# Optimization experiments

Hardware: AMD Instinct MI355X
Metric: run time of the kernel (lower is better)

The kernel has to match this reference:

```python
import jax, jax.numpy as jnp
import numpy as np

VOCAB = 10000
KEY_SIZE = 256
VALUE_SIZE = 256
HIDDEN = KEY_SIZE + VALUE_SIZE  # 512, embedding dim (tied with output head)
SOS = 33


def _lstm_cell(x, h, c, W_ih, W_hh, b_ih, b_hh):
    # torch.nn.LSTMCell: gates = x@W_ih^T + b_ih + h@W_hh^T + b_hh, order i,f,g,o
    g = x @ W_ih.T + b_ih + h @ W_hh.T + b_hh
    i, f, gg, o = jnp.split(g, 4, axis=1)
    c_new = jax.nn.sigmoid(f) * c + jax.nn.sigmoid(i) * jnp.tanh(gg)
    h_new = jax.nn.sigmoid(o) * jnp.tanh(c_new)
    return h_new, c_new


def _attend(q, K, V, invalid):
    # q: [N,H]; K: [N,T,H]; V: [N,T,Vd]; invalid: [N,T] bool mask of padded positions
    energy = jnp.einsum('nth,nh->nt', K, q)
    energy = jnp.where(invalid, jnp.float32(-1e10), energy)
    attn = jax.nn.softmax(energy, axis=1)
    ctx = jnp.einsum('nt,ntv->nv', attn, V)
    return ctx


def setup_inputs() -> dict:
    key0 = jax.random.key(0)
    ks = jax.random.split(key0, 16)
    N, T, L = 64, 512, 256
    values = jax.random.normal(ks[0], (N, T, VALUE_SIZE), dtype=jnp.float32)
    key = jax.random.normal(ks[1], (N, T, KEY_SIZE), dtype=jnp.float32)
    lens = jax.random.randint(ks[2], (N,), 64, T + 1, dtype=jnp.int32)
    text = jax.random.randint(ks[3], (N, L), 0, VOCAB, dtype=jnp.int32)
    s = 1.0 / np.sqrt(KEY_SIZE)
    E = jax.random.normal(ks[4], (VOCAB, HIDDEN), dtype=jnp.float32) * 0.02
    b_out = jnp.zeros((VOCAB,), dtype=jnp.float32)
    W_ih1 = jax.random.uniform(ks[5], (4 * KEY_SIZE, HIDDEN + VALUE_SIZE), jnp.float32, -s, s)
    W_hh1 = jax.random.uniform(ks[6], (4 * KEY_SIZE, KEY_SIZE), jnp.float32, -s, s)
    b_ih1 = jax.random.uniform(ks[7], (4 * KEY_SIZE,), jnp.float32, -s, s)
    b_hh1 = jax.random.uniform(ks[8], (4 * KEY_SIZE,), jnp.float32, -s, s)
    W_ih2 = jax.random.uniform(ks[9], (4 * KEY_SIZE, KEY_SIZE), jnp.float32, -s, s)
    W_hh2 = jax.random.uniform(ks[10], (4 * KEY_SIZE, KEY_SIZE), jnp.float32, -s, s)
    b_ih2 = jax.random.uniform(ks[11], (4 * KEY_SIZE,), jnp.float32, -s, s)
    b_hh2 = jax.random.uniform(ks[12], (4 * KEY_SIZE,), jnp.float32, -s, s)
    return {"values": values, "key": key, "lens": lens, "text": text,
            "E": E, "b_out": b_out,
            "W_ih1": W_ih1, "W_hh1": W_hh1, "b_ih1": b_ih1, "b_hh1": b_hh1,
            "W_ih2": W_ih2, "W_hh2": W_hh2, "b_ih2": b_ih2, "b_hh2": b_hh2}


def reference(values, key, lens, text, E, b_out,
              W_ih1, W_hh1, b_ih1, b_hh1, W_ih2, W_hh2, b_ih2, b_hh2):
    # isAttended=True, isTrain=True, teacher_force_rate=1.0 -> always teacher forcing.
    N, T, _ = values.shape
    L = text.shape[1]
    invalid = jnp.arange(T)[None, :] >= lens[:, None]  # [N,T] padded positions

    # char embeddings fed at each step: step 0 uses <sos>=33, step i>0 uses text[:, i-1]
    emb = E[text]                                   # [N,L,H]
    first = jnp.broadcast_to(E[SOS][None, :], (N, HIDDEN))
    emb_seq = jnp.concatenate([first[None], jnp.swapaxes(emb, 0, 1)[:-1]], axis=0)  # [L,N,H]

    ctx0 = _attend(jnp.zeros((N, KEY_SIZE), values.dtype), key, values, invalid)
    h1 = jnp.zeros((N, KEY_SIZE), values.dtype)
    carry0 = (h1, h1, h1, h1, ctx0)  # (h1,c1,h2,c2,context)

    def step(carry, char_embed):
        h1, c1, h2, c2, ctx = carry
        inp = jnp.concatenate([char_embed, ctx], axis=1)   # [N, H+V]
        h1, c1 = _lstm_cell(inp, h1, c1, W_ih1, W_hh1, b_ih1, b_hh1)
        h2, c2 = _lstm_cell(h1, h2, c2, W_ih2, W_hh2, b_ih2, b_hh2)
        ctx = _attend(h2, key, values, invalid)
        logits = jnp.concatenate([h2, ctx], axis=1) @ E.T + b_out  # tied weights
        return (h1, c1, h2, c2, ctx), logits

    _, preds = jax.lax.scan(step, carry0, emb_seq)  # [L,N,VOCAB]
    return jnp.transpose(preds, (1, 0, 2))          # [N,L,VOCAB]
```

## Files before the change

kernel.cpp:

```cpp
#include <hip/hip_runtime.h>
#include <hip/hip_bf16.h>
#include <math.h>

#define NB     64
#define TT     512
#define KS     256
#define VS     256
#define HID    512
#define GATES  1024
#define LL     256
#define VOC    10000
#define SOSTOK 33

__device__ __forceinline__ float sigmoidf_(float x) { return 1.0f / (1.0f + expf(-x)); }

__global__ __launch_bounds__(256)
void pack_kernel(const float* __restrict__ W_ih1, const float* __restrict__ W_hh1,
                 const float* __restrict__ b_ih1, const float* __restrict__ b_hh1,
                 const float* __restrict__ W_ih2, const float* __restrict__ W_hh2,
                 const float* __restrict__ b_ih2, const float* __restrict__ b_hh2,
                 float* __restrict__ W1T, float* __restrict__ W2T,
                 float* __restrict__ b1s, float* __restrict__ b2s)
{
    int idx = blockIdx.x * 256 + threadIdx.x;
    if (idx < 512 * 1024) {
        int k = idx >> 10;
        int j = idx & 1023;
        W1T[idx] = (k < 256) ? W_ih1[j * 768 + 512 + k] : W_hh1[j * 256 + (k - 256)];
        W2T[idx] = (k < 256) ? W_ih2[j * 256 + k]       : W_hh2[j * 256 + (k - 256)];
    }
    if (idx < 1024) {
        b1s[idx] = b_ih1[idx] + b_hh1[idx];
        b2s[idx] = b_ih2[idx] + b_hh2[idx];
    }
}

template <int MODE>
__global__ __launch_bounds__(256)
void gemm_nt(const float* __restrict__ A, const float* __restrict__ B,
             float* __restrict__ C, const float* __restrict__ bias,
             int M, int Nn, int K, int lda, int ldb, int ldc)
{
    const int BM = 128, BN = 128, BK = 16;
    __shared__ float As[BK][BM + 4];
    __shared__ float Bs[BK][BN + 4];

    const int m0 = blockIdx.y * BM;
    const int n0 = blockIdx.x * BN;
    const int tid = threadIdx.x;
    const int tx = tid & 15;
    const int ty = tid >> 4;
    const int lr = tid >> 2;
    const int lq = tid & 3;

    float acc[8][8];
#pragma unroll
    for (int i = 0; i < 8; i++)
#pragma unroll
        for (int j = 0; j < 8; j++) acc[i][j] = 0.0f;

    for (int k0 = 0; k0 < K; k0 += BK) {
#pragma unroll
        for (int h = 0; h < 2; h++) {
            int r = lr + h * 64;
            int gm = m0 + r;
            float4 v = make_float4(0.f, 0.f, 0.f, 0.f);
            if (gm < M) v = *(const float4*)(A + (size_t)gm * lda + k0 + lq * 4);
            As[lq * 4 + 0][r] = v.x; As[lq * 4 + 1][r] = v.y;
            As[lq * 4 + 2][r] = v.z; As[lq * 4 + 3][r] = v.w;
        }
#pragma unroll
        for (int h = 0; h < 2; h++) {
            int r = lr + h * 64;
            int gn = n0 + r;
            float4 v = make_float4(0.f, 0.f, 0.f, 0.f);
            if (gn < Nn) v = *(const float4*)(B + (size_t)gn * ldb + k0 + lq * 4);
            Bs[lq * 4 + 0][r] = v.x; Bs[lq * 4 + 1][r] = v.y;
            Bs[lq * 4 + 2][r] = v.z; Bs[lq * 4 + 3][r] = v.w;
        }
        __syncthreads();

#pragma unroll
        for (int kk = 0; kk < BK; kk++) {
            float a[8], b[8];
            *(float4*)&a[0] = *(const float4*)&As[kk][ty * 4];
            *(float4*)&a[4] = *(const float4*)&As[kk][64 + ty * 4];
            *(float4*)&b[0] = *(const float4*)&Bs[kk][tx * 4];
            *(float4*)&b[4] = *(const float4*)&Bs[kk][64 + tx * 4];
#pragma unroll
            for (int i = 0; i < 8; i++)
#pragma unroll
                for (int j = 0; j < 8; j++) acc[i][j] += a[i] * b[j];
        }
        __syncthreads();
    }

    int row[8];
#pragma unroll
    for (int i = 0; i < 8; i++) row[i] = m0 + ((i < 4) ? (ty * 4 + i) : (64 + ty * 4 + (i - 4)));
    const int c0 = n0 + tx * 4;
    const int c1 = n0 + 64 + tx * 4;

    if (MODE == 0) {
#pragma unroll
        for (int i = 0; i < 8; i++) {
            if (row[i] >= M) continue;
            float* cp = C + (size_t)row[i] * ldc;
#pragma unroll
            for (int jh = 0; jh < 2; jh++) {
                int cc = jh ? c1 : c0;
                if (cc + 3 < Nn) {
                    *(float4*)(cp + cc) = make_float4(acc[i][jh * 4 + 0], acc[i][jh * 4 + 1],
                                                      acc[i][jh * 4 + 2], acc[i][jh * 4 + 3]);
                } else {
                    for (int j = 0; j < 4; j++)
                        if (cc + j < Nn) cp[cc + j] = acc[i][jh * 4 + j];
                }
            }
        }
    } else {
        float bv0[4], bv1[4];
#pragma unroll
        for (int j = 0; j < 4; j++) {
            bv0[j] = (c0 + j < Nn) ? bias[c0 + j] : 0.f;
            bv1[j] = (c1 + j < Nn) ? bias[c1 + j] : 0.f;
        }
#pragma unroll
        for (int i = 0; i < 8; i++) {
            int m = row[i];
            int t = m >> 6;
            int nb = m & 63;
            float* cp = C + ((size_t)nb * LL + t) * VOC;
#pragma unroll
            for (int jh = 0; jh < 2; jh++) {
                int cc = jh ? c1 : c0;
                float* bv = jh ? bv1 : bv0;
                if (cc + 3 < Nn) {
                    *(float4*)(cp + cc) = make_float4(acc[i][jh * 4 + 0] + bv[0],
                                                      acc[i][jh * 4 + 1] + bv[1],
                                                      acc[i][jh * 4 + 2] + bv[2],
                                                      acc[i][jh * 4 + 3] + bv[3]);
                } else {
                    for (int j = 0; j < 4; j++)
                        if (cc + j < Nn) cp[cc + j] = acc[i][jh * 4 + j] + bv[j];
                }
            }
        }
    }
}

__global__ __launch_bounds__(256)
void seq_kernel(const float* __restrict__ Vmat,
                const float* __restrict__ Kmat,
                const int* __restrict__ lens,
                const int* __restrict__ text,
                const float* __restrict__ preE,
                const float* __restrict__ W1T,
                const float* __restrict__ W2T,
                const float* __restrict__ b1s,
                const float* __restrict__ b2s,
                float* __restrict__ S)
{
    const int n = blockIdx.x;
    const int tid = threadIdx.x;

    __shared__ float h1[KS], c1v[KS], h2[KS], c2v[KS], ctx[VS];
    __shared__ float xv[512];
    __shared__ float attn[TT];
    __shared__ float red[256];

    const int len = lens[n];
    const float* Kn = Kmat + (size_t)n * TT * KS;
    const float* Vn = Vmat + (size_t)n * TT * VS;

    h1[tid] = 0.f; c1v[tid] = 0.f; h2[tid] = 0.f; c2v[tid] = 0.f;
    __syncthreads();

    auto attention = [&]() {
        float e0 = -1e10f, e1 = -1e10f;
        {
            int t = tid;
            if (t < len) {
                const float4* kr = (const float4*)(Kn + (size_t)t * KS);
                float acc = 0.f;
#pragma unroll 8
                for (int k4 = 0; k4 < KS / 4; k4++) {
                    float4 kv = kr[k4];
                    acc += kv.x * h2[k4 * 4 + 0];
                    acc += kv.y * h2[k4 * 4 + 1];
                    acc += kv.z * h2[k4 * 4 + 2];
                    acc += kv.w * h2[k4 * 4 + 3];
                }
                e0 = acc;
            }
            t = tid + 256;
            if (t < len) {
                const float4* kr = (const float4*)(Kn + (size_t)t * KS);
                float acc = 0.f;
#pragma unroll 8
                for (int k4 = 0; k4 < KS / 4; k4++) {
                    float4 kv = kr[k4];
                    acc += kv.x * h2[k4 * 4 + 0];
                    acc += kv.y * h2[k4 * 4 + 1];
                    acc += kv.z * h2[k4 * 4 + 2];
                    acc += kv.w * h2[k4 * 4 + 3];
                }
                e1 = acc;
            }
        }
        red[tid] = fmaxf(e0, e1);
        __syncthreads();
#pragma unroll
        for (int s = 128; s > 0; s >>= 1) {
            if (tid < s) red[tid] = fmaxf(red[tid], red[tid + s]);
            __syncthreads();
        }
        float M = red[0];
        __syncthreads();
        float p0 = expf(e0 - M);
        float p1 = expf(e1 - M);
        attn[tid] = p0; attn[tid + 256] = p1;
        red[tid] = p0 + p1;
        __syncthreads();
#pragma unroll
        for (int s = 128; s > 0; s >>= 1) {
            if (tid < s) red[tid] += red[tid + s];
            __syncthreads();
        }
        float inv = 1.0f / red[0];
        float acc = 0.f;
        const float* vb = Vn + tid;
        for (int t = 0; t < len; t++) acc += attn[t] * vb[(size_t)t * VS];
        ctx[tid] = acc * inv;
        __syncthreads();
    };

    auto lstm = [&](const float* __restrict__ WT, const float* __restrict__ bsum,
                    const float* __restrict__ pre, float* hs, float* cs,
                    const float* xa, const float* xb) {
        xv[tid] = xa[tid];
        xv[256 + tid] = xb[tid];
        __syncthreads();
        float a0 = 0.f, a1 = 0.f, a2 = 0.f, a3 = 0.f;
#pragma unroll 8
        for (int k = 0; k < 512; k++) {
            float x = xv[k];
            const float* wr = WT + (k << 10) + tid;
            a0 += x * wr[0];
            a1 += x * wr[256];
            a2 += x * wr[512];
            a3 += x * wr[768];
        }
        float gi = a0 + bsum[tid];
        float gf = a1 + bsum[tid + 256];
        float gg = a2 + bsum[tid + 512];
        float go = a3 + bsum[tid + 768];
        if (pre) {
            gi += pre[tid];
            gf += pre[tid + 256];
            gg += pre[tid + 512];
            go += pre[tid + 768];
        }
        float c = sigmoidf_(gf) * cs[tid] + sigmoidf_(gi) * tanhf(gg);
        float h = sigmoidf_(go) * tanhf(c);
        __syncthreads();
        hs[tid] = h;
        cs[tid] = c;
        __syncthreads();
    };

    attention();

    for (int t = 0; t < LL; t++) {
        int tok = (t == 0) ? SOSTOK : text[n * LL + (t - 1)];
        lstm(W1T, b1s, preE + (size_t)tok * GATES, h1, c1v, ctx, h1);
        lstm(W2T, b2s, (const float*)nullptr,      h2, c2v, h1, h2);
        attention();
        float* srow = S + ((size_t)t * NB + n) * HID;
        srow[tid] = h2[tid];
        srow[256 + tid] = ctx[tid];
    }
}

extern "C" void kernel_launch(void* const* d_in, const int* in_sizes, int n_in,
                              void* d_out, int out_size, void* d_ws, size_t ws_size,
                              hipStream_t stream)
{
    const float* values = (const float*)d_in[0];
    const float* key    = (const float*)d_in[1];
    const int*   lens   = (const int*)d_in[2];
    const int*   text   = (const int*)d_in[3];
    const float* E      = (const float*)d_in[4];
    const float* b_out  = (const float*)d_in[5];
    const float* W_ih1  = (const float*)d_in[6];
    const float* W_hh1  = (const float*)d_in[7];
    const float* b_ih1  = (const float*)d_in[8];
    const float* b_hh1  = (const float*)d_in[9];
    const float* W_ih2  = (const float*)d_in[10];
    const float* W_hh2  = (const float*)d_in[11];
    const float* b_ih2  = (const float*)d_in[12];
    const float* b_hh2  = (const float*)d_in[13];

    float* ws   = (float*)d_ws;
    float* W1T  = ws;
    float* W2T  = W1T + 524288;
    float* b1s  = W2T + 524288;
    float* b2s  = b1s + 1024;
    float* preE = b2s + 1024;
    float* S    = preE + 10240000;
    float* out  = (float*)d_out;

    hipLaunchKernelGGL(pack_kernel, dim3(2048), dim3(256), 0, stream,
                       W_ih1, W_hh1, b_ih1, b_hh1, W_ih2, W_hh2, b_ih2, b_hh2,
                       W1T, W2T, b1s, b2s);

    hipLaunchKernelGGL((gemm_nt<0>), dim3(8, 79), dim3(256), 0, stream,
                       E, W_ih1, preE, (const float*)nullptr,
                       10000, 1024, 512, 512, 768, 1024);

    hipLaunchKernelGGL(seq_kernel, dim3(64), dim3(256), 0, stream,
                       values, key, lens, text, preE, W1T, W2T, b1s, b2s, S);

    hipLaunchKernelGGL((gemm_nt<1>), dim3(79, 128), dim3(256), 0, stream,
                       S, E, out, b_out,
                       16384, 10000, 512, 512, 512, 0);
}
```

Baseline: 25.88 ms.

## Split sequential decoder across 256 cooperative blocks with group barriers and split-softmax attention

Replaces the 64-block recurrent kernel, one block per batch item, with a 256-block cooperative kernel. Each group of 64 blocks owns 16 batch rows and a slice of LSTM gate columns, and keeps its weight slice resident in shared memory. Attention is split into four time quarters per row and combined with a log-sum-exp merge through global scratch and atomics. The aim is to use far more CUs and stop re-streaming the LSTM weights from global memory every step. In exchange it adds custom global barriers, three per step, and extra global traffic for the h1 and context exchange.

Measured after the change: 49.50 ms. 1.91x slower.

```diff
diff --git a/kernel.cpp b/kernel.cpp
--- a/kernel.cpp
+++ b/kernel.cpp
@@ -1,5 +1,4 @@
 #include <hip/hip_runtime.h>
-#include <hip/hip_bf16.h>
 #include <math.h>
 
 #define NB     64
@@ -12,6 +11,10 @@
 #define VOC    10000
 #define SOSTOK 33
 
+#define NBLK   256
+#define GBLK   64
+#define NTHR   256
+
 __device__ __forceinline__ float sigmoidf_(float x) { return 1.0f / (1.0f + expf(-x)); }
 
 __global__ __launch_bounds__(256)
@@ -19,20 +22,23 @@
                  const float* __restrict__ b_ih1, const float* __restrict__ b_hh1,
                  const float* __restrict__ W_ih2, const float* __restrict__ W_hh2,
                  const float* __restrict__ b_ih2, const float* __restrict__ b_hh2,
-                 float* __restrict__ W1T, float* __restrict__ W2T,
-                 float* __restrict__ b1s, float* __restrict__ b2s)
+                 float* __restrict__ W1c, float* __restrict__ W2c,
+                 float* __restrict__ b1s, float* __restrict__ b2s,
+                 unsigned* __restrict__ cnt, unsigned* __restrict__ bars)
 {
     int idx = blockIdx.x * 256 + threadIdx.x;
-    if (idx < 512 * 1024) {
-        int k = idx >> 10;
-        int j = idx & 1023;
-        W1T[idx] = (k < 256) ? W_ih1[j * 768 + 512 + k] : W_hh1[j * 256 + (k - 256)];
-        W2T[idx] = (k < 256) ? W_ih2[j * 256 + k]       : W_hh2[j * 256 + (k - 256)];
+    if (idx < 1024 * 512) {
+        int j = idx >> 9;
+        int k = idx & 511;
+        W1c[idx] = (k < 256) ? W_ih1[j * 768 + 512 + k] : W_hh1[j * 256 + (k - 256)];
+        W2c[idx] = (k < 256) ? W_ih2[j * 256 + k]       : W_hh2[j * 256 + (k - 256)];
     }
     if (idx < 1024) {
         b1s[idx] = b_ih1[idx] + b_hh1[idx];
         b2s[idx] = b_ih2[idx] + b_hh2[idx];
-    }
+        cnt[idx] = 0u;
+    }
+    if (idx < 256) bars[idx] = 0u;
 }
 
 template <int MODE>
@@ -149,136 +155,256 @@
     }
 }
 
-__global__ __launch_bounds__(256)
-void seq_kernel(const float* __restrict__ Vmat,
-                const float* __restrict__ Kmat,
-                const int* __restrict__ lens,
-                const int* __restrict__ text,
-                const float* __restrict__ preE,
-                const float* __restrict__ W1T,
-                const float* __restrict__ W2T,
-                const float* __restrict__ b1s,
-                const float* __restrict__ b2s,
-                float* __restrict__ S)
+__device__ __forceinline__ void group_sync(unsigned* cntp, unsigned* genp)
 {
-    const int n = blockIdx.x;
+    __threadfence();
+    __syncthreads();
+    if (threadIdx.x == 0) {
+        unsigned g = __hip_atomic_load(genp, __ATOMIC_RELAXED, __HIP_MEMORY_SCOPE_AGENT);
+        unsigned old = __hip_atomic_fetch_add(cntp, 1u, __ATOMIC_RELAXED, __HIP_MEMORY_SCOPE_AGENT);
+        if (old == GBLK - 1) {
+            __hip_atomic_store(cntp, 0u, __ATOMIC_RELAXED, __HIP_MEMORY_SCOPE_AGENT);
+            __hip_atomic_store(genp, g + 1u, __ATOMIC_RELEASE, __HIP_MEMORY_SCOPE_AGENT);
+        } else {
+            unsigned cur;
+            do {
+                __builtin_amdgcn_s_sleep(2);
+                cur = __hip_atomic_load(genp, __ATOMIC_RELAXED, __HIP_MEMORY_SCOPE_AGENT);
+            } while (cur == g);
+        }
+    }
+    __syncthreads();
+    __threadfence();
+}
+
+__global__ __launch_bounds__(256, 1)
+void seq_coop(const float* __restrict__ Vmat,
+              const float* __restrict__ Kmat,
+              const int* __restrict__ lens,
+              const int* __restrict__ text,
+              const float* __restrict__ preE,
+              const float* __restrict__ W1c,
+              const float* __restrict__ W2c,
+              const float* __restrict__ b1s,
+              const float* __restrict__ b2s,
+              float* __restrict__ S,
+              float* __restrict__ h1buf,
+              float* __restrict__ ctxbuf,
+              float* __restrict__ am,
+              float* __restrict__ as_,
+              float* __restrict__ actxp,
+              unsigned* __restrict__ cnt,
+              unsigned* __restrict__ bars)
+{
+    __shared__ float ws1[16][516];
+    __shared__ float ws2[16][516];
+    __shared__ float xs [16][516];
+    __shared__ float gl [16][16];
+    __shared__ float red[256];
+    __shared__ float h2s[256];
+    __shared__ float pl [128];
+    __shared__ float cred[4][64][4];
+    __shared__ int   flagv;
+
+    const int b   = blockIdx.x;
     const int tid = threadIdx.x;
-
-    __shared__ float h1[KS], c1v[KS], h2[KS], c2v[KS], ctx[VS];
-    __shared__ float xv[512];
-    __shared__ float attn[TT];
-    __shared__ float red[256];
-
-    const int len = lens[n];
-    const float* Kn = Kmat + (size_t)n * TT * KS;
-    const float* Vn = Vmat + (size_t)n * TT * VS;
-
-    h1[tid] = 0.f; c1v[tid] = 0.f; h2[tid] = 0.f; c2v[tid] = 0.f;
-    __syncthreads();
-
-    auto attention = [&]() {
-        float e0 = -1e10f, e1 = -1e10f;
+    const int grp = b >> 6;
+    const int n0  = grp * 16;
+    const int ct  = b & 63;
+    const int na  = n0 + ((b >> 2) & 15);
+    const int q   = b & 3;
+    const int t0a = q * 128;
+    unsigned* cntp = bars + grp * 64;
+    unsigned* genp = bars + grp * 64 + 32;
+
+    const int sub = tid & 15;
+    const int nl  = tid >> 4;
+    const int g4  = sub >> 2;
+    const int cl  = sub & 3;
+    const int jj  = g4 * 256 + ct * 4 + cl;
+
+    for (int i = tid; i < 2048; i += 256) {
+        int r = i >> 7, k4 = i & 127;
+        int j = (r >> 2) * 256 + ct * 4 + (r & 3);
+        *(float4*)&ws1[r][k4 * 4] = *(const float4*)(W1c + (size_t)j * 512 + k4 * 4);
+        *(float4*)&ws2[r][k4 * 4] = *(const float4*)(W2c + (size_t)j * 512 + k4 * 4);
+    }
+    const float b1r = b1s[jj];
+    const float b2r = b2s[jj];
+    const int len_att = lens[na];
+    float c1reg = 0.f, c2reg = 0.f;
+
+    for (int t = -1; t < LL; ++t) {
+        if (t >= 0) {
+            const int p = t & 1;
+            for (int i = tid; i < 2048; i += 256) {
+                int inl = i >> 7, k4 = i & 127;
+                int n = n0 + inl;
+                float4 v;
+                if (k4 < 64)      v = *(const float4*)(ctxbuf + n * 256 + k4 * 4);
+                else if (t == 0)  v = make_float4(0.f, 0.f, 0.f, 0.f);
+                else              v = *(const float4*)(h1buf + (p ^ 1) * NB * 256 + n * 256 + (k4 - 64) * 4);
+                *(float4*)&xs[inl][k4 * 4] = v;
+            }
+            __syncthreads();
+            {
+                int n = n0 + nl;
+                int tok = (t == 0) ? SOSTOK : text[n * LL + (t - 1)];
+                float pre = preE[(size_t)tok * GATES + jj];
+                float4 a4 = make_float4(0.f, 0.f, 0.f, 0.f);
+                const float* wr = &ws1[sub][0];
+                const float* xr = &xs[nl][0];
+#pragma unroll 8
+                for (int k4 = 0; k4 < 128; k4++) {
+                    float4 w  = *(const float4*)(wr + k4 * 4);
+                    float4 xv = *(const float4*)(xr + k4 * 4);
+                    a4.x += w.x * xv.x; a4.y += w.y * xv.y;
+                    a4.z += w.z * xv.z; a4.w += w.w * xv.w;
+                }
+                gl[nl][sub] = (a4.x + a4.y) + (a4.z + a4.w) + b1r + pre;
+            }
+            __syncthreads();
+            if (tid < 64) {
+                int unl = tid >> 2, ucl = tid & 3;
+                float gi = gl[unl][ucl],     gf = gl[unl][4 + ucl];
+                float gg = gl[unl][8 + ucl], go = gl[unl][12 + ucl];
+                float c = sigmoidf_(gf) * c1reg + sigmoidf_(gi) * tanhf(gg);
+                float h = sigmoidf_(go) * tanhf(c);
+                c1reg = c;
+                h1buf[p * NB * 256 + (n0 + unl) * 256 + (ct * 4 + ucl)] = h;
+            }
+            group_sync(cntp, genp);
+
+            for (int i = tid; i < 2048; i += 256) {
+                int inl = i >> 7, k4 = i & 127;
+                int n = n0 + inl;
+                float4 v;
+                if (k4 < 64)      v = *(const float4*)(h1buf + p * NB * 256 + n * 256 + k4 * 4);
+                else if (t == 0)  v = make_float4(0.f, 0.f, 0.f, 0.f);
+                else              v = *(const float4*)(S + ((size_t)(t - 1) * NB + n) * HID + (k4 - 64) * 4);
+                *(float4*)&xs[inl][k4 * 4] = v;
+            }
+            __syncthreads();
+            {
+                float4 a4 = make_float4(0.f, 0.f, 0.f, 0.f);
+                const float* wr = &ws2[sub][0];
+                const float* xr = &xs[nl][0];
+#pragma unroll 8
+                for (int k4 = 0; k4 < 128; k4++) {
+                    float4 w  = *(const float4*)(wr + k4 * 4);
+                    float4 xv = *(const float4*)(xr + k4 * 4);
+                    a4.x += w.x * xv.x; a4.y += w.y * xv.y;
+                    a4.z += w.z * xv.z; a4.w += w.w * xv.w;
+                }
+                gl[nl][sub] = (a4.x + a4.y) + (a4.z + a4.w) + b2r;
+            }
+            __syncthreads();
+            if (tid < 64) {
+                int unl = tid >> 2, ucl = tid & 3;
+                float gi = gl[unl][ucl],     gf = gl[unl][4 + ucl];
+                float gg = gl[unl][8 + ucl], go = gl[unl][12 + ucl];
+                float c = sigmoidf_(gf) * c2reg + sigmoidf_(gi) * tanhf(gg);
+                float h = sigmoidf_(go) * tanhf(c);
+                c2reg = c;
+                S[((size_t)t * NB + (n0 + unl)) * HID + (ct * 4 + ucl)] = h;
+            }
+            group_sync(cntp, genp);
+        }
+
+        h2s[tid] = (t < 0) ? 0.f : S[((size_t)t * NB + na) * HID + tid];
+        __syncthreads();
         {
-            int t = tid;
-            if (t < len) {
-                const float4* kr = (const float4*)(Kn + (size_t)t * KS);
-                float acc = 0.f;
+            int tl = tid >> 1, kh = tid & 1;
+            int tg = t0a + tl;
+            float e = 0.f;
+            if (tg < len_att) {
+                const float4* kr = (const float4*)(Kmat + ((size_t)na * TT + tg) * KS) + kh * 32;
+                const float4* hh = ((const float4*)h2s) + kh * 32;
 #pragma unroll 8
-                for (int k4 = 0; k4 < KS / 4; k4++) {
-                    float4 kv = kr[k4];
-                    acc += kv.x * h2[k4 * 4 + 0];
-                    acc += kv.y * h2[k4 * 4 + 1];
-                    acc += kv.z * h2[k4 * 4 + 2];
-                    acc += kv.w * h2[k4 * 4 + 3];
+                for (int k4 = 0; k4 < 32; k4++) {
+                    float4 kv = kr[k4], hv = hh[k4];
+                    e += kv.x * hv.x + kv.y * hv.y + kv.z * hv.z + kv.w * hv.w;
                 }
-                e0 = acc;
-            }
-            t = tid + 256;
-            if (t < len) {
-                const float4* kr = (const float4*)(Kn + (size_t)t * KS);
-                float acc = 0.f;
-#pragma unroll 8
-                for (int k4 = 0; k4 < KS / 4; k4++) {
-                    float4 kv = kr[k4];
-                    acc += kv.x * h2[k4 * 4 + 0];
-                    acc += kv.y * h2[k4 * 4 + 1];
-                    acc += kv.z * h2[k4 * 4 + 2];
-                    acc += kv.w * h2[k4 * 4 + 3];
-                }
-                e1 = acc;
-            }
-        }
-        red[tid] = fmaxf(e0, e1);
-        __syncthreads();
-#pragma unroll
+            }
+            red[tid] = e;
+        }
+        __syncthreads();
+        if (tid < 128) {
+            int tg = t0a + tid;
+            float ef = (tg < len_att) ? (red[2 * tid] + red[2 * tid + 1]) : -1e30f;
+            pl[tid] = ef;
+        }
+        __syncthreads();
+        red[tid] = (tid < 128) ? pl[tid] : -1e30f;
+        __syncthreads();
         for (int s = 128; s > 0; s >>= 1) {
             if (tid < s) red[tid] = fmaxf(red[tid], red[tid + s]);
             __syncthreads();
         }
-        float M = red[0];
-        __syncthreads();
-        float p0 = expf(e0 - M);
-        float p1 = expf(e1 - M);
-        attn[tid] = p0; attn[tid + 256] = p1;
-        red[tid] = p0 + p1;
-        __syncthreads();
-#pragma unroll
+        float mq = red[0];
+        __syncthreads();
+        {
+            float pv = 0.f;
+            if (tid < 128 && (t0a + tid) < len_att) pv = expf(pl[tid] - mq);
+            if (tid < 128) pl[tid] = pv;
+            red[tid] = pv;
+        }
+        __syncthreads();
         for (int s = 128; s > 0; s >>= 1) {
             if (tid < s) red[tid] += red[tid + s];
             __syncthreads();
         }
-        float inv = 1.0f / red[0];
-        float acc = 0.f;
-        const float* vb = Vn + tid;
-        for (int t = 0; t < len; t++) acc += attn[t] * vb[(size_t)t * VS];
-        ctx[tid] = acc * inv;
-        __syncthreads();
-    };
-
-    auto lstm = [&](const float* __restrict__ WT, const float* __restrict__ bsum,
-                    const float* __restrict__ pre, float* hs, float* cs,
-                    const float* xa, const float* xb) {
-        xv[tid] = xa[tid];
-        xv[256 + tid] = xb[tid];
-        __syncthreads();
-        float a0 = 0.f, a1 = 0.f, a2 = 0.f, a3 = 0.f;
-#pragma unroll 8
-        for (int k = 0; k < 512; k++) {
-            float x = xv[k];
-            const float* wr = WT + (k << 10) + tid;
-            a0 += x * wr[0];
-            a1 += x * wr[256];
-            a2 += x * wr[512];
-            a3 += x * wr[768];
-        }
-        float gi = a0 + bsum[tid];
-        float gf = a1 + bsum[tid + 256];
-        float gg = a2 + bsum[tid + 512];
-        float go = a3 + bsum[tid + 768];
-        if (pre) {
-            gi += pre[tid];
-            gf += pre[tid + 256];
-            gg += pre[tid + 512];
-            go += pre[tid + 768];
-        }
-        float c = sigmoidf_(gf) * cs[tid] + sigmoidf_(gi) * tanhf(gg);
-        float h = sigmoidf_(go) * tanhf(c);
-        __syncthreads();
-        hs[tid] = h;
-        cs[tid] = c;
-        __syncthreads();
-    };
-
-    attention();
-
-    for (int t = 0; t < LL; t++) {
-        int tok = (t == 0) ? SOSTOK : text[n * LL + (t - 1)];
-        lstm(W1T, b1s, preE + (size_t)tok * GATES, h1, c1v, ctx, h1);
-        lstm(W2T, b2s, (const float*)nullptr,      h2, c2v, h1, h2);
-        attention();
-        float* srow = S + ((size_t)t * NB + n) * HID;
-        srow[tid] = h2[tid];
-        srow[256 + tid] = ctx[tid];
+        float sq = red[0];
+        __syncthreads();
+        {
+            int tq = tid >> 6, v4 = tid & 63;
+            float4 a = make_float4(0.f, 0.f, 0.f, 0.f);
+            int tlim = len_att - t0a;
+            int tend = min(tq * 32 + 32, tlim);
+            for (int tl = tq * 32; tl < tend; tl++) {
+                float p_ = pl[tl];
+                float4 vv = *(const float4*)(Vmat + ((size_t)na * TT + t0a + tl) * VS + v4 * 4);
+                a.x += p_ * vv.x; a.y += p_ * vv.y; a.z += p_ * vv.z; a.w += p_ * vv.w;
+            }
+            cred[tq][v4][0] = a.x; cred[tq][v4][1] = a.y;
+            cred[tq][v4][2] = a.z; cred[tq][v4][3] = a.w;
+        }
+        __syncthreads();
+        {
+            int v4 = tid >> 2, comp = tid & 3;
+            float sum = cred[0][v4][comp] + cred[1][v4][comp]
+                      + cred[2][v4][comp] + cred[3][v4][comp];
+            actxp[(size_t)(na * 4 + q) * 256 + tid] = sum;
+        }
+        if (tid == 0) { am[na * 4 + q] = mq; as_[na * 4 + q] = sq; }
+        __threadfence();
+        __syncthreads();
+        if (tid == 0) {
+            unsigned old = __hip_atomic_fetch_add(&cnt[na * 16], 1u,
+                                                  __ATOMIC_RELAXED, __HIP_MEMORY_SCOPE_AGENT);
+            flagv = (old == 3u) ? 1 : 0;
+        }
+        __syncthreads();
+        if (flagv) {
+            __threadfence();
+            float m0 = am[na * 4 + 0], m1 = am[na * 4 + 1];
+            float m2 = am[na * 4 + 2], m3 = am[na * 4 + 3];
+            float M = fmaxf(fmaxf(m0, m1), fmaxf(m2, m3));
+            float w0 = expf(m0 - M), w1 = expf(m1 - M);
+            float w2 = expf(m2 - M), w3 = expf(m3 - M);
+            float denom = as_[na * 4 + 0] * w0 + as_[na * 4 + 1] * w1
+                        + as_[na * 4 + 2] * w2 + as_[na * 4 + 3] * w3;
+            float inv = 1.0f / denom;
+            float cv = (actxp[(size_t)(na * 4 + 0) * 256 + tid] * w0
+                      + actxp[(size_t)(na * 4 + 1) * 256 + tid] * w1
+                      + actxp[(size_t)(na * 4 + 2) * 256 + tid] * w2
+                      + actxp[(size_t)(na * 4 + 3) * 256 + tid] * w3) * inv;
+            ctxbuf[na * 256 + tid] = cv;
+            if (t >= 0) S[((size_t)t * NB + na) * HID + 256 + tid] = cv;
+            if (tid == 0)
+                __hip_atomic_store(&cnt[na * 16], 0u, __ATOMIC_RELAXED, __HIP_MEMORY_SCOPE_AGENT);
+        }
+        group_sync(cntp, genp);
     }
 }
 
@@ -301,25 +427,35 @@
     const float* b_ih2  = (const float*)d_in[12];
     const float* b_hh2  = (const float*)d_in[13];
 
-    float* ws   = (float*)d_ws;
-    float* W1T  = ws;
-    float* W2T  = W1T + 524288;
-    float* b1s  = W2T + 524288;
-    float* b2s  = b1s + 1024;
-    float* preE = b2s + 1024;
-    float* S    = preE + 10240000;
-    float* out  = (float*)d_out;
+    float* ws     = (float*)d_ws;
+    float* W1c    = ws;
+    float* W2c    = W1c + 524288;
+    float* b1s    = W2c + 524288;
+    float* b2s    = b1s + 1024;
+    float* preE   = b2s + 1024;
+    float* S      = preE + 10240000;
+    float* h1buf  = S + 8388608;
+    float* ctxbuf = h1buf + 32768;
+    float* am     = ctxbuf + 16384;
+    float* as_    = am + 256;
+    float* actxp  = as_ + 256;
+    unsigned* cnt  = (unsigned*)(actxp + 65536);
+    unsigned* bars = cnt + 1024;
+    float* out    = (float*)d_out;
 
     hipLaunchKernelGGL(pack_kernel, dim3(2048), dim3(256), 0, stream,
                        W_ih1, W_hh1, b_ih1, b_hh1, W_ih2, W_hh2, b_ih2, b_hh2,
-                       W1T, W2T, b1s, b2s);
+                       W1c, W2c, b1s, b2s, cnt, bars);
 
     hipLaunchKernelGGL((gemm_nt<0>), dim3(8, 79), dim3(256), 0, stream,
                        E, W_ih1, preE, (const float*)nullptr,
                        10000, 1024, 512, 512, 768, 1024);
 
-    hipLaunchKernelGGL(seq_kernel, dim3(64), dim3(256), 0, stream,
-                       values, key, lens, text, preE, W1T, W2T, b1s, b2s, S);
+    void* args[] = {(void*)&values, (void*)&key, (void*)&lens, (void*)&text,
+                    (void*)&preE, (void*)&W1c, (void*)&W2c, (void*)&b1s, (void*)&b2s,
+                    (void*)&S, (void*)&h1buf, (void*)&ctxbuf, (void*)&am, (void*)&as_,
+                    (void*)&actxp, (void*)&cnt, (void*)&bars};
+    hipLaunchCooperativeKernel((void*)seq_coop, dim3(NBLK), dim3(NTHR), args, 0, stream);
 
     hipLaunchKernelGGL((gemm_nt<1>), dim3(79, 128), dim3(256), 0, stream,
                        S, E, out, b_out,
```
